# Performance work log

Measured on AMD Instinct MI355X. Metric: run time of the kernel, lower is better.

Reference implementation:

```python
import jax, jax.numpy as jnp
import numpy as np

BATCH, VOCAB = 256, 50257

def setup_inputs() -> dict:
    key = jax.random.key(0)
    k1, k2 = jax.random.split(key)
    logits = jax.random.normal(k1, (BATCH, VOCAB), dtype=jnp.float32) * 4.0  # LM-like logit spread
    temperature = jax.random.uniform(k2, (), dtype=jnp.float32, minval=0.5, maxval=1.5)
    return {"logits": logits, "temperature": temperature, "top_k": 50}


def reference(logits, temperature, top_k):
    # temperature scale (dividing by 1.0 is identical to the torch skip-branch)
    scaled = logits / temperature
    # top-k mask: keep exactly the k selected positions, -inf elsewhere
    top_vals, top_idx = jax.lax.top_k(scaled, top_k)          # [B, k]
    b = jnp.arange(scaled.shape[0])[:, None]                  # [B, 1]
    masked = jnp.full_like(scaled, -jnp.inf).at[b, top_idx].set(top_vals)
    # softmax + multinomial(num_samples=1) == categorical over masked logits
    key = jax.random.key(42)
    sampled = jax.random.categorical(key, masked, axis=-1)    # [B]
    return sampled
```

## Files before the change

### kernel.cpp

```cpp
#include <hip/hip_runtime.h>
#include <stdint.h>


#define VOCAB 50257
#define BATCH 256
#define NT 1024
#define NTF 256
#define NSEG 16
#define SEG4 786
#define CAP_SEG 64
#define NBINS 4096
#define HBINS 1024
#define BSHIFT 15
#define BCAP 256
#define CAND_CAP 2048
#define FILTER_VAL 4.0f
#define SPEC_VAL 10.0f

__device__ __forceinline__ uint32_t rotl32(uint32_t v, int r) {
  return (v << r) | (v >> (32 - r));
}

__device__ __forceinline__ void threefry2x32_42(uint32_t& x0, uint32_t& x1) {
  const uint32_t ks0 = 0u;
  const uint32_t ks1 = 42u;
  const uint32_t ks2 = ks0 ^ ks1 ^ 0x1BD11BDAu;
  x0 += ks0; x1 += ks1;
#define TF_R(r) { x0 += x1; x1 = rotl32(x1, (r)); x1 ^= x0; }
  TF_R(13) TF_R(15) TF_R(26) TF_R(6)
  x0 += ks1; x1 += ks2 + 1u;
  TF_R(17) TF_R(29) TF_R(16) TF_R(24)
  x0 += ks2; x1 += ks0 + 2u;
  TF_R(13) TF_R(15) TF_R(26) TF_R(6)
  x0 += ks0; x1 += ks1 + 3u;
  TF_R(17) TF_R(29) TF_R(16) TF_R(24)
  x0 += ks1; x1 += ks2 + 4u;
  TF_R(13) TF_R(15) TF_R(26) TF_R(6)
  x0 += ks2; x1 += ks0 + 5u;
#undef TF_R
}

__device__ __forceinline__ float gumbel_at(uint32_t flat) {
  uint32_t x0 = 0u, x1 = flat;
  threefry2x32_42(x0, x1);
  uint32_t bits = x0 ^ x1;
  uint32_t fb = (bits >> 9) | 0x3f800000u;
  float f = __uint_as_float(fb) - 1.0f;
  float u = fmaxf(f, 1.17549435e-38f);
  float t = (float)log((double)u);
  float g = (float)(-log((double)(-t)));
  return g;
}

__device__ __forceinline__ uint32_t fkey(float x) {
  uint32_t u = __float_as_uint(x);
  return (u & 0x80000000u) ? ~u : (u | 0x80000000u);
}

__device__ __forceinline__ float inv_fkey(uint32_t k) {
  uint32_t u = (k & 0x80000000u) ? (k ^ 0x80000000u) : ~k;
  return __uint_as_float(u);
}

extern "C" __global__ void __launch_bounds__(NTF)
filter_kernel(const float* __restrict__ logits,
              int* __restrict__ cnt,
              int* __restrict__ cand) {
  const int b = blockIdx.x;
  const int row = b >> 4;
  const int seg = b & 15;
  const int tid = threadIdx.x;
  const float* rowp = logits + (size_t)row * VOCAB;

  const int pc = (4 - (row & 3)) & 3;
  const int nv4 = (VOCAB - pc) >> 2;
  const int tailbase = pc + (nv4 << 2);
  const int tailc = VOCAB - tailbase;
  const float4* body = (const float4*)(rowp + pc);

  __shared__ int lcnt;
  if (tid == 0) lcnt = 0;
  __syncthreads();

  int* myc = cand + (b << 6);
  const int st = seg * SEG4;
  const int en = min(nv4, st + SEG4);
  for (int v = st + tid; v < en; v += NTF) {
    float4 x = body[v];
    int base = pc + (v << 2);
    if (x.x >= SPEC_VAL) { int p = atomicAdd(&lcnt, 1); if (p < CAP_SEG) myc[p] = base; }
    if (x.y >= SPEC_VAL) { int p = atomicAdd(&lcnt, 1); if (p < CAP_SEG) myc[p] = base + 1; }
    if (x.z >= SPEC_VAL) { int p = atomicAdd(&lcnt, 1); if (p < CAP_SEG) myc[p] = base + 2; }
    if (x.w >= SPEC_VAL) { int p = atomicAdd(&lcnt, 1); if (p < CAP_SEG) myc[p] = base + 3; }
  }
  if (seg == 0 && tid < pc) {
    if (rowp[tid] >= SPEC_VAL) { int p = atomicAdd(&lcnt, 1); if (p < CAP_SEG) myc[p] = tid; }
  }
  if (seg == NSEG - 1 && tid < tailc) {
    if (rowp[tailbase + tid] >= SPEC_VAL) {
      int p = atomicAdd(&lcnt, 1); if (p < CAP_SEG) myc[p] = tailbase + tid;
    }
  }
  __syncthreads();
  if (tid == 0) cnt[b] = lcnt;
}

extern "C" __global__ void __launch_bounds__(NTF)
refine_kernel(const float* __restrict__ logits,
              const float* __restrict__ temp_p,
              const int* __restrict__ topk_p,
              int* __restrict__ out,
              const int* __restrict__ cnt,
              const int* __restrict__ cand,
              int* __restrict__ flags) {
  const int row = blockIdx.x;
  const int tid = threadIdx.x;
  const int lane = tid & 63;
  const int wave = tid >> 6;

  __shared__ int scnt[NSEG], soff[NSEG];
  __shared__ int sh_total, sh_ok, sh_tb, sh_need, sh_bcnt;
  __shared__ unsigned ckey[CAND_CAP];
  __shared__ int cidx[CAND_CAP];
  __shared__ unsigned hist[HBINS];
  __shared__ unsigned bkey[BCAP];
  __shared__ int bidx[BCAP];
  __shared__ unsigned wtot[4], aboveWave[4];
  __shared__ float wbv[4];
  __shared__ int wbi[4];

  const int K = topk_p[0];
  const float temp = temp_p[0];

  if (tid < NSEG) scnt[tid] = cnt[(row << 4) + tid];
  if (tid == 0) { sh_ok = 0; sh_bcnt = 0; }
  for (int b = tid; b < HBINS; b += NTF) hist[b] = 0u;
  __syncthreads();
  if (tid == 0) {
    int acc = 0, ovf = 0;
    for (int s = 0; s < NSEG; ++s) {
      soff[s] = acc;
      if (scnt[s] > CAP_SEG) ovf = 1;
      acc += scnt[s];
    }
    sh_total = ovf ? -1 : acc;
  }
  __syncthreads();
  const int total = sh_total;

  if (!(total >= K && total <= CAND_CAP)) {
    if (tid == 0) flags[row] = 0;
    return;
  }

  {
    int s = tid >> 4, j0 = tid & 15;
    const int* src = cand + (((row << 4) + s) << 6);
    for (int j = j0; j < scnt[s]; j += 16) cidx[soff[s] + j] = src[j];
  }
  __syncthreads();

  const float* rowp = logits + (size_t)row * VOCAB;
  const uint32_t cutkey = fkey(SPEC_VAL / temp);
  for (int c = tid; c < total; c += NTF) {
    unsigned k = fkey(rowp[cidx[c]] / temp);
    ckey[c] = k;
    unsigned bin = min((unsigned)(HBINS - 1), (k - cutkey) >> BSHIFT);
    atomicAdd(&hist[bin], 1u);
  }
  __syncthreads();

  {
    unsigned p = hist[4 * tid] + hist[4 * tid + 1] + hist[4 * tid + 2] + hist[4 * tid + 3];
    unsigned vv = p;
    for (int off = 1; off < 64; off <<= 1) {
      unsigned o = (unsigned)__shfl_down((int)vv, off);
      if (lane + off < 64) vv += o;
    }
    if (lane == 0) wtot[wave] = vv;
    __syncthreads();
    if (tid == 0) {
      unsigned acc = 0;
      for (int w = 3; w >= 0; --w) { aboveWave[w] = acc; acc += wtot[w]; }
    }
    __syncthreads();
    unsigned above = aboveWave[wave] + (vv - p);
    if (above < (unsigned)K && above + p >= (unsigned)K) {
      int need = K - (int)above;
      for (int b = 3; b >= 0; --b) {
        unsigned c = hist[4 * tid + b];
        if (c >= (unsigned)need) { sh_tb = 4 * tid + b; sh_need = need; break; }
        need -= (int)c;
      }
    }
  }
  __syncthreads();
  const int tb = sh_tb;
  const int need = sh_need;

  for (int c = tid; c < total; c += NTF) {
    unsigned k = ckey[c];
    unsigned bin = min((unsigned)(HBINS - 1), (k - cutkey) >> BSHIFT);
    if ((int)bin == tb) {
      int p = atomicAdd(&sh_bcnt, 1);
      if (p < BCAP) { bkey[p] = k; bidx[p] = cidx[c]; }
    }
  }
  __syncthreads();
  const int m = sh_bcnt;
  if (m > BCAP) {
    if (tid == 0) flags[row] = 0;
    return;
  }

  float bestv = -__builtin_huge_valf();
  int besti = 0x7fffffff;

  if (tid < m) {
    const unsigned mk = bkey[tid];
    const int mi = bidx[tid];
    int rank = 0;
    for (int j = 0; j < m; ++j) {
      unsigned k = bkey[j];
      rank += (k > mk || (k == mk && bidx[j] < mi)) ? 1 : 0;
    }
    if (rank == need - 1) {
      sh_ok = (tb > 0 || mk > cutkey) ? 1 : 0;
    }
    if (rank < need) {
      float s = inv_fkey(mk);
      float v = s + gumbel_at((uint32_t)row * (uint32_t)VOCAB + (uint32_t)mi);
      if (v > bestv || (v == bestv && mi < besti)) { bestv = v; besti = mi; }
    }
  }

  for (int c = tid; c < total; c += NTF) {
    unsigned k = ckey[c];
    unsigned bin = min((unsigned)(HBINS - 1), (k - cutkey) >> BSHIFT);
    if ((int)bin > tb) {
      int mi = cidx[c];
      float s = inv_fkey(k);
      float v = s + gumbel_at((uint32_t)row * (uint32_t)VOCAB + (uint32_t)mi);
      if (v > bestv || (v == bestv && mi < besti)) { bestv = v; besti = mi; }
    }
  }
  __syncthreads();
  if (!sh_ok) {
    if (tid == 0) flags[row] = 0;
    return;
  }

  for (int off = 32; off > 0; off >>= 1) {
    float v2 = __shfl_down(bestv, off);
    int i2 = __shfl_down(besti, off);
    if (v2 > bestv || (v2 == bestv && i2 < besti)) { bestv = v2; besti = i2; }
  }
  if (lane == 0) { wbv[wave] = bestv; wbi[wave] = besti; }
  __syncthreads();
  if (tid == 0) {
    float bv = wbv[0]; int bi = wbi[0];
    for (int w = 1; w < 4; ++w) {
      if (wbv[w] > bv || (wbv[w] == bv && wbi[w] < bi)) { bv = wbv[w]; bi = wbi[w]; }
    }
    out[row] = bi;
    flags[row] = 1;
  }
}

extern "C" __global__ void __launch_bounds__(NT)
fallback_kernel(const float* __restrict__ logits,
                const float* __restrict__ temp_p,
                const int* __restrict__ topk_p,
                int* __restrict__ out,
                const int* __restrict__ flags) {
  const int row = blockIdx.x;
  if (flags[row]) return;

  const int tid = threadIdx.x;
  const float temp = temp_p[0];
  const int K = topk_p[0];
  const float* rowp = logits + (size_t)row * VOCAB;

  const int pc = (4 - (row & 3)) & 3;
  const int nv4 = (VOCAB - pc) >> 2;
  const int tailbase = pc + (nv4 << 2);
  const int tailc = VOCAB - tailbase;
  const float4* body = (const float4*)(rowp + pc);

  __shared__ unsigned hist[NBINS];
  __shared__ unsigned wtot[16];
  __shared__ unsigned aboveWave[16];
  __shared__ int sh_tb, sh_total, sh_cnt;
  __shared__ unsigned ckey[CAND_CAP];
  __shared__ int cidx[CAND_CAP];
  __shared__ float wbv[16];
  __shared__ int wbi[16];

  const int lane = tid & 63;
  const int wave = tid >> 6;

  float bestv = -__builtin_huge_valf();
  int besti = 0x7fffffff;

  uint32_t filt = fkey(FILTER_VAL);
  int tb = 0;
  for (;;) {
    for (int b = tid; b < NBINS; b += NT) hist[b] = 0u;
    __syncthreads();
    if (tid < pc) {
      uint32_t k = fkey(rowp[tid]);
      if (k >= filt) atomicAdd(&hist[k >> 20], 1u);
    }
    for (int w = tid; w < nv4; w += NT) {
      float4 x = body[w];
      uint32_t k0 = fkey(x.x), k1 = fkey(x.y), k2 = fkey(x.z), k3 = fkey(x.w);
      if (k0 >= filt) atomicAdd(&hist[k0 >> 20], 1u);
      if (k1 >= filt) atomicAdd(&hist[k1 >> 20], 1u);
      if (k2 >= filt) atomicAdd(&hist[k2 >> 20], 1u);
      if (k3 >= filt) atomicAdd(&hist[k3 >> 20], 1u);
    }
    if (tid < tailc) {
      uint32_t k = fkey(rowp[tailbase + tid]);
      if (k >= filt) atomicAdd(&hist[k >> 20], 1u);
    }
    __syncthreads();

    unsigned p = hist[4 * tid] + hist[4 * tid + 1] + hist[4 * tid + 2] + hist[4 * tid + 3];
    unsigned vv = p;
    for (int off = 1; off < 64; off <<= 1) {
      unsigned o = (unsigned)__shfl_down((int)vv, off);
      if (lane + off < 64) vv += o;
    }
    if (lane == 0) wtot[wave] = vv;
    __syncthreads();
    if (tid == 0) {
      unsigned acc = 0;
      for (int w = 15; w >= 0; --w) { aboveWave[w] = acc; acc += wtot[w]; }
      sh_total = (int)acc;
    }
    __syncthreads();
    unsigned above = aboveWave[wave] + (vv - p);
    if (above < (unsigned)K && above + p >= (unsigned)K) {
      int need = K - (int)above;
      for (int b = 3; b >= 0; --b) {
        unsigned c = hist[4 * tid + b];
        if (c >= (unsigned)need) { sh_tb = 4 * tid + b; break; }
        need -= (int)c;
      }
    }
    __syncthreads();
    if (sh_total >= K) { tb = sh_tb; break; }
    filt = 0u;
    __syncthreads();
  }

  const uint32_t cutk = (uint32_t)max(tb - 1, 0) << 20;
  if (tid == 0) sh_cnt = 0;
  __syncthreads();
  if (tid < pc) {
    if (fkey(rowp[tid]) >= cutk) {
      int p = atomicAdd(&sh_cnt, 1);
      if (p < CAND_CAP) cidx[p] = tid;
    }
  }
  for (int w = tid; w < nv4; w += NT) {
    float4 x = body[w];
    int base = pc + (w << 2);
    if (fkey(x.x) >= cutk) { int p = atomicAdd(&sh_cnt, 1); if (p < CAND_CAP) cidx[p] = base; }
    if (fkey(x.y) >= cutk) { int p = atomicAdd(&sh_cnt, 1); if (p < CAND_CAP) cidx[p] = base + 1; }
    if (fkey(x.z) >= cutk) { int p = atomicAdd(&sh_cnt, 1); if (p < CAND_CAP) cidx[p] = base + 2; }
    if (fkey(x.w) >= cutk) { int p = atomicAdd(&sh_cnt, 1); if (p < CAND_CAP) cidx[p] = base + 3; }
  }
  if (tid < tailc) {
    if (fkey(rowp[tailbase + tid]) >= cutk) {
      int p = atomicAdd(&sh_cnt, 1);
      if (p < CAND_CAP) cidx[p] = tailbase + tid;
    }
  }
  __syncthreads();
  const int C = min(sh_cnt, CAND_CAP);

  if (tid < C) {
    int idx = cidx[tid];
    float s = rowp[idx] / temp;
    ckey[tid] = fkey(s);
  }
  __syncthreads();

  if (tid < C) {
    const uint32_t mk = ckey[tid];
    const int mi = cidx[tid];
    int rank = 0;
    for (int j = 0; j < C; ++j) {
      uint32_t k = ckey[j];
      rank += (k > mk || (k == mk && cidx[j] < mi)) ? 1 : 0;
    }
    if (rank < K) {
      float s = rowp[mi] / temp;
      float v2 = s + gumbel_at((uint32_t)row * (uint32_t)VOCAB + (uint32_t)mi);
      bestv = v2; besti = mi;
    }
  }
  __syncthreads();

  for (int off = 32; off > 0; off >>= 1) {
    float v2 = __shfl_down(bestv, off);
    int i2 = __shfl_down(besti, off);
    if (v2 > bestv || (v2 == bestv && i2 < besti)) { bestv = v2; besti = i2; }
  }
  if (lane == 0) { wbv[wave] = bestv; wbi[wave] = besti; }
  __syncthreads();
  if (tid == 0) {
    float bv = wbv[0];
    int bi = wbi[0];
    for (int w = 1; w < 16; ++w) {
      if (wbv[w] > bv || (wbv[w] == bv && wbi[w] < bi)) { bv = wbv[w]; bi = wbi[w]; }
    }
    out[row] = bi;
  }
}

extern "C" void kernel_launch(void* const* d_in, const int* in_sizes, int n_in,
                              void* d_out, int out_size, void* d_ws, size_t ws_size,
                              hipStream_t stream) {
  const float* logits = (const float*)d_in[0];
  const float* temp_p = (const float*)d_in[1];
  const int* topk_p = (const int*)d_in[2];
  int* out = (int*)d_out;

  int* cnt = (int*)d_ws;
  int* cand = cnt + BATCH * NSEG;
  int* flags = cand + BATCH * NSEG * CAP_SEG;

  hipLaunchKernelGGL(filter_kernel, dim3(BATCH * NSEG), dim3(NTF), 0, stream,
                     logits, cnt, cand);
  hipLaunchKernelGGL(refine_kernel, dim3(BATCH), dim3(NTF), 0, stream,
                     logits, temp_p, topk_p, out, cnt, cand, flags);
  hipLaunchKernelGGL(fallback_kernel, dim3(BATCH), dim3(NT), 0, stream,
                     logits, temp_p, topk_p, out, flags);
}
```

Before: 95.80 us.

## Merge fallback into refine kernel and store candidate values alongside indices

The filter kernel now writes each candidate's logit value next to its index, so the refine step no longer gathers from the full logits row. The fallback path is folded into the refine kernel, which now runs with 1024 threads and uses a 1024-bin histogram with one bin per thread. This removes the third kernel launch and the flags buffer. In exchange the refine blocks are larger and carry more shared memory on every row, and the filter kernel writes twice as much to the workspace.

```diff
diff --git a/kernel.cpp b/kernel.cpp
--- a/kernel.cpp
+++ b/kernel.cpp
@@ -65,7 +65,8 @@
 extern "C" __global__ void __launch_bounds__(NTF)
 filter_kernel(const float* __restrict__ logits,
               int* __restrict__ cnt,
-              int* __restrict__ cand) {
+              int* __restrict__ cand_idx,
+              float* __restrict__ cand_val) {
   const int b = blockIdx.x;
   const int row = b >> 4;
   const int seg = b & 15;
@@ -82,59 +83,62 @@
   if (tid == 0) lcnt = 0;
   __syncthreads();
 
-  int* myc = cand + (b << 6);
+  int* myi = cand_idx + (b << 6);
+  float* myv = cand_val + (b << 6);
   const int st = seg * SEG4;
   const int en = min(nv4, st + SEG4);
   for (int v = st + tid; v < en; v += NTF) {
     float4 x = body[v];
     int base = pc + (v << 2);
-    if (x.x >= SPEC_VAL) { int p = atomicAdd(&lcnt, 1); if (p < CAP_SEG) myc[p] = base; }
-    if (x.y >= SPEC_VAL) { int p = atomicAdd(&lcnt, 1); if (p < CAP_SEG) myc[p] = base + 1; }
-    if (x.z >= SPEC_VAL) { int p = atomicAdd(&lcnt, 1); if (p < CAP_SEG) myc[p] = base + 2; }
-    if (x.w >= SPEC_VAL) { int p = atomicAdd(&lcnt, 1); if (p < CAP_SEG) myc[p] = base + 3; }
+    if (x.x >= SPEC_VAL) { int p = atomicAdd(&lcnt, 1); if (p < CAP_SEG) { myi[p] = base;     myv[p] = x.x; } }
+    if (x.y >= SPEC_VAL) { int p = atomicAdd(&lcnt, 1); if (p < CAP_SEG) { myi[p] = base + 1; myv[p] = x.y; } }
+    if (x.z >= SPEC_VAL) { int p = atomicAdd(&lcnt, 1); if (p < CAP_SEG) { myi[p] = base + 2; myv[p] = x.z; } }
+    if (x.w >= SPEC_VAL) { int p = atomicAdd(&lcnt, 1); if (p < CAP_SEG) { myi[p] = base + 3; myv[p] = x.w; } }
   }
   if (seg == 0 && tid < pc) {
-    if (rowp[tid] >= SPEC_VAL) { int p = atomicAdd(&lcnt, 1); if (p < CAP_SEG) myc[p] = tid; }
+    float x = rowp[tid];
+    if (x >= SPEC_VAL) { int p = atomicAdd(&lcnt, 1); if (p < CAP_SEG) { myi[p] = tid; myv[p] = x; } }
   }
   if (seg == NSEG - 1 && tid < tailc) {
-    if (rowp[tailbase + tid] >= SPEC_VAL) {
-      int p = atomicAdd(&lcnt, 1); if (p < CAP_SEG) myc[p] = tailbase + tid;
+    float x = rowp[tailbase + tid];
+    if (x >= SPEC_VAL) {
+      int p = atomicAdd(&lcnt, 1); if (p < CAP_SEG) { myi[p] = tailbase + tid; myv[p] = x; }
     }
   }
   __syncthreads();
   if (tid == 0) cnt[b] = lcnt;
 }
 
-extern "C" __global__ void __launch_bounds__(NTF)
+extern "C" __global__ void __launch_bounds__(NT)
 refine_kernel(const float* __restrict__ logits,
               const float* __restrict__ temp_p,
               const int* __restrict__ topk_p,
               int* __restrict__ out,
               const int* __restrict__ cnt,
-              const int* __restrict__ cand,
-              int* __restrict__ flags) {
+              const int* __restrict__ cand_idx,
+              const float* __restrict__ cand_val) {
   const int row = blockIdx.x;
   const int tid = threadIdx.x;
   const int lane = tid & 63;
   const int wave = tid >> 6;
 
-  __shared__ int scnt[NSEG], soff[NSEG];
-  __shared__ int sh_total, sh_ok, sh_tb, sh_need, sh_bcnt;
+  __shared__ unsigned hist[NBINS];
   __shared__ unsigned ckey[CAND_CAP];
   __shared__ int cidx[CAND_CAP];
-  __shared__ unsigned hist[HBINS];
+  __shared__ int scnt[NSEG], soff[NSEG];
+  __shared__ int sh_total, sh_ok, sh_tb, sh_need, sh_bcnt, sh_cnt;
   __shared__ unsigned bkey[BCAP];
   __shared__ int bidx[BCAP];
-  __shared__ unsigned wtot[4], aboveWave[4];
-  __shared__ float wbv[4];
-  __shared__ int wbi[4];
+  __shared__ unsigned wtot[16], aboveWave[16];
+  __shared__ float wbv[16];
+  __shared__ int wbi[16];
 
   const int K = topk_p[0];
   const float temp = temp_p[0];
 
   if (tid < NSEG) scnt[tid] = cnt[(row << 4) + tid];
   if (tid == 0) { sh_ok = 0; sh_bcnt = 0; }
-  for (int b = tid; b < HBINS; b += NTF) hist[b] = 0u;
+  if (tid < HBINS) hist[tid] = 0u;
   __syncthreads();
   if (tid == 0) {
     int acc = 0, ovf = 0;
@@ -148,275 +152,242 @@
   __syncthreads();
   const int total = sh_total;
 
-  if (!(total >= K && total <= CAND_CAP)) {
-    if (tid == 0) flags[row] = 0;
-    return;
-  }
-
-  {
-    int s = tid >> 4, j0 = tid & 15;
-    const int* src = cand + (((row << 4) + s) << 6);
-    for (int j = j0; j < scnt[s]; j += 16) cidx[soff[s] + j] = src[j];
-  }
-  __syncthreads();
-
-  const float* rowp = logits + (size_t)row * VOCAB;
+  int ok = (total >= K && total <= CAND_CAP) ? 1 : 0;
   const uint32_t cutkey = fkey(SPEC_VAL / temp);
-  for (int c = tid; c < total; c += NTF) {
-    unsigned k = fkey(rowp[cidx[c]] / temp);
-    ckey[c] = k;
-    unsigned bin = min((unsigned)(HBINS - 1), (k - cutkey) >> BSHIFT);
-    atomicAdd(&hist[bin], 1u);
-  }
-  __syncthreads();
-
-  {
-    unsigned p = hist[4 * tid] + hist[4 * tid + 1] + hist[4 * tid + 2] + hist[4 * tid + 3];
-    unsigned vv = p;
-    for (int off = 1; off < 64; off <<= 1) {
-      unsigned o = (unsigned)__shfl_down((int)vv, off);
-      if (lane + off < 64) vv += o;
-    }
-    if (lane == 0) wtot[wave] = vv;
-    __syncthreads();
-    if (tid == 0) {
-      unsigned acc = 0;
-      for (int w = 3; w >= 0; --w) { aboveWave[w] = acc; acc += wtot[w]; }
-    }
-    __syncthreads();
-    unsigned above = aboveWave[wave] + (vv - p);
-    if (above < (unsigned)K && above + p >= (unsigned)K) {
-      int need = K - (int)above;
-      for (int b = 3; b >= 0; --b) {
-        unsigned c = hist[4 * tid + b];
-        if (c >= (unsigned)need) { sh_tb = 4 * tid + b; sh_need = need; break; }
-        need -= (int)c;
-      }
-    }
-  }
-  __syncthreads();
-  const int tb = sh_tb;
-  const int need = sh_need;
-
-  for (int c = tid; c < total; c += NTF) {
-    unsigned k = ckey[c];
-    unsigned bin = min((unsigned)(HBINS - 1), (k - cutkey) >> BSHIFT);
-    if ((int)bin == tb) {
-      int p = atomicAdd(&sh_bcnt, 1);
-      if (p < BCAP) { bkey[p] = k; bidx[p] = cidx[c]; }
-    }
-  }
-  __syncthreads();
-  const int m = sh_bcnt;
-  if (m > BCAP) {
-    if (tid == 0) flags[row] = 0;
-    return;
-  }
 
   float bestv = -__builtin_huge_valf();
   int besti = 0x7fffffff;
 
-  if (tid < m) {
-    const unsigned mk = bkey[tid];
-    const int mi = bidx[tid];
-    int rank = 0;
-    for (int j = 0; j < m; ++j) {
-      unsigned k = bkey[j];
-      rank += (k > mk || (k == mk && bidx[j] < mi)) ? 1 : 0;
-    }
-    if (rank == need - 1) {
-      sh_ok = (tb > 0 || mk > cutkey) ? 1 : 0;
-    }
-    if (rank < need) {
-      float s = inv_fkey(mk);
-      float v = s + gumbel_at((uint32_t)row * (uint32_t)VOCAB + (uint32_t)mi);
-      if (v > bestv || (v == bestv && mi < besti)) { bestv = v; besti = mi; }
-    }
-  }
-
-  for (int c = tid; c < total; c += NTF) {
-    unsigned k = ckey[c];
-    unsigned bin = min((unsigned)(HBINS - 1), (k - cutkey) >> BSHIFT);
-    if ((int)bin > tb) {
-      int mi = cidx[c];
-      float s = inv_fkey(k);
-      float v = s + gumbel_at((uint32_t)row * (uint32_t)VOCAB + (uint32_t)mi);
-      if (v > bestv || (v == bestv && mi < besti)) { bestv = v; besti = mi; }
-    }
-  }
-  __syncthreads();
-  if (!sh_ok) {
-    if (tid == 0) flags[row] = 0;
+  if (ok) {
+    {
+      int s = tid >> 6, j0 = tid & 63;
+      const int* srci = cand_idx + (((row << 4) + s) << 6);
+      const float* srcv = cand_val + (((row << 4) + s) << 6);
+      for (int j = j0; j < scnt[s]; j += 64) {
+        int o = soff[s] + j;
+        cidx[o] = srci[j];
+        ckey[o] = fkey(srcv[j] / temp);
+      }
+    }
+    __syncthreads();
+    for (int c = tid; c < total; c += NT) {
+      unsigned bin = min((unsigned)(HBINS - 1), (ckey[c] - cutkey) >> BSHIFT);
+      atomicAdd(&hist[bin], 1u);
+    }
+    __syncthreads();
+    {
+      unsigned p = hist[tid];
+      unsigned vv = p;
+      for (int off = 1; off < 64; off <<= 1) {
+        unsigned o = (unsigned)__shfl_down((int)vv, off);
+        if (lane + off < 64) vv += o;
+      }
+      if (lane == 0) wtot[wave] = vv;
+      __syncthreads();
+      if (tid == 0) {
+        unsigned acc = 0;
+        for (int w = 15; w >= 0; --w) { aboveWave[w] = acc; acc += wtot[w]; }
+      }
+      __syncthreads();
+      unsigned above = aboveWave[wave] + (vv - p);
+      if (above < (unsigned)K && above + p >= (unsigned)K) {
+        sh_tb = tid; sh_need = K - (int)above;
+      }
+    }
+    __syncthreads();
+    const int tb = sh_tb;
+    const int need = sh_need;
+
+    for (int c = tid; c < total; c += NT) {
+      unsigned k = ckey[c];
+      unsigned bin = min((unsigned)(HBINS - 1), (k - cutkey) >> BSHIFT);
+      if ((int)bin == tb) {
+        int p = atomicAdd(&sh_bcnt, 1);
+        if (p < BCAP) { bkey[p] = k; bidx[p] = cidx[c]; }
+      }
+    }
+    __syncthreads();
+    const int m = sh_bcnt;
+    if (m > BCAP) ok = 0;
+
+    if (ok) {
+      if (tid < m) {
+        const unsigned mk = bkey[tid];
+        const int mi = bidx[tid];
+        int rank = 0;
+        for (int j = 0; j < m; ++j) {
+          unsigned k = bkey[j];
+          rank += (k > mk || (k == mk && bidx[j] < mi)) ? 1 : 0;
+        }
+        if (rank == need - 1) {
+          sh_ok = (tb > 0 || mk > cutkey) ? 1 : 0;
+        }
+        if (rank < need) {
+          float s = inv_fkey(mk);
+          float v = s + gumbel_at((uint32_t)row * (uint32_t)VOCAB + (uint32_t)mi);
+          if (v > bestv || (v == bestv && mi < besti)) { bestv = v; besti = mi; }
+        }
+      }
+      for (int c = tid; c < total; c += NT) {
+        unsigned k = ckey[c];
+        unsigned bin = min((unsigned)(HBINS - 1), (k - cutkey) >> BSHIFT);
+        if ((int)bin > tb) {
+          int mi = cidx[c];
+          float s = inv_fkey(k);
+          float v = s + gumbel_at((uint32_t)row * (uint32_t)VOCAB + (uint32_t)mi);
+          if (v > bestv || (v == bestv && mi < besti)) { bestv = v; besti = mi; }
+        }
+      }
+      __syncthreads();
+      if (!sh_ok) ok = 0;
+    }
+  }
+
+  if (ok) {
+    for (int off = 32; off > 0; off >>= 1) {
+      float v2 = __shfl_down(bestv, off);
+      int i2 = __shfl_down(besti, off);
+      if (v2 > bestv || (v2 == bestv && i2 < besti)) { bestv = v2; besti = i2; }
+    }
+    if (lane == 0) { wbv[wave] = bestv; wbi[wave] = besti; }
+    __syncthreads();
+    if (tid == 0) {
+      float bv = wbv[0]; int bi = wbi[0];
+      for (int w = 1; w < 16; ++w) {
+        if (wbv[w] > bv || (wbv[w] == bv && wbi[w] < bi)) { bv = wbv[w]; bi = wbi[w]; }
+      }
+      out[row] = bi;
+    }
     return;
   }
 
-  for (int off = 32; off > 0; off >>= 1) {
-    float v2 = __shfl_down(bestv, off);
-    int i2 = __shfl_down(besti, off);
-    if (v2 > bestv || (v2 == bestv && i2 < besti)) { bestv = v2; besti = i2; }
-  }
-  if (lane == 0) { wbv[wave] = bestv; wbi[wave] = besti; }
-  __syncthreads();
-  if (tid == 0) {
-    float bv = wbv[0]; int bi = wbi[0];
-    for (int w = 1; w < 4; ++w) {
-      if (wbv[w] > bv || (wbv[w] == bv && wbi[w] < bi)) { bv = wbv[w]; bi = wbi[w]; }
-    }
-    out[row] = bi;
-    flags[row] = 1;
-  }
-}
-
-extern "C" __global__ void __launch_bounds__(NT)
-fallback_kernel(const float* __restrict__ logits,
-                const float* __restrict__ temp_p,
-                const int* __restrict__ topk_p,
-                int* __restrict__ out,
-                const int* __restrict__ flags) {
-  const int row = blockIdx.x;
-  if (flags[row]) return;
-
-  const int tid = threadIdx.x;
-  const float temp = temp_p[0];
-  const int K = topk_p[0];
-  const float* rowp = logits + (size_t)row * VOCAB;
-
-  const int pc = (4 - (row & 3)) & 3;
-  const int nv4 = (VOCAB - pc) >> 2;
-  const int tailbase = pc + (nv4 << 2);
-  const int tailc = VOCAB - tailbase;
-  const float4* body = (const float4*)(rowp + pc);
-
-  __shared__ unsigned hist[NBINS];
-  __shared__ unsigned wtot[16];
-  __shared__ unsigned aboveWave[16];
-  __shared__ int sh_tb, sh_total, sh_cnt;
-  __shared__ unsigned ckey[CAND_CAP];
-  __shared__ int cidx[CAND_CAP];
-  __shared__ float wbv[16];
-  __shared__ int wbi[16];
-
-  const int lane = tid & 63;
-  const int wave = tid >> 6;
-
-  float bestv = -__builtin_huge_valf();
-  int besti = 0x7fffffff;
-
-  uint32_t filt = fkey(FILTER_VAL);
-  int tb = 0;
-  for (;;) {
-    for (int b = tid; b < NBINS; b += NT) hist[b] = 0u;
+  {
+    const float* rowp = logits + (size_t)row * VOCAB;
+    const int pc = (4 - (row & 3)) & 3;
+    const int nv4 = (VOCAB - pc) >> 2;
+    const int tailbase = pc + (nv4 << 2);
+    const int tailc = VOCAB - tailbase;
+    const float4* body = (const float4*)(rowp + pc);
+
+    bestv = -__builtin_huge_valf();
+    besti = 0x7fffffff;
+
+    uint32_t filt = fkey(FILTER_VAL);
+    int tb = 0;
+    for (;;) {
+      for (int b = tid; b < NBINS; b += NT) hist[b] = 0u;
+      __syncthreads();
+      if (tid < pc) {
+        uint32_t k = fkey(rowp[tid]);
+        if (k >= filt) atomicAdd(&hist[k >> 20], 1u);
+      }
+      for (int w = tid; w < nv4; w += NT) {
+        float4 x = body[w];
+        uint32_t k0 = fkey(x.x), k1 = fkey(x.y), k2 = fkey(x.z), k3 = fkey(x.w);
+        if (k0 >= filt) atomicAdd(&hist[k0 >> 20], 1u);
+        if (k1 >= filt) atomicAdd(&hist[k1 >> 20], 1u);
+        if (k2 >= filt) atomicAdd(&hist[k2 >> 20], 1u);
+        if (k3 >= filt) atomicAdd(&hist[k3 >> 20], 1u);
+      }
+      if (tid < tailc) {
+        uint32_t k = fkey(rowp[tailbase + tid]);
+        if (k >= filt) atomicAdd(&hist[k >> 20], 1u);
+      }
+      __syncthreads();
+
+      unsigned p = hist[4 * tid] + hist[4 * tid + 1] + hist[4 * tid + 2] + hist[4 * tid + 3];
+      unsigned vv = p;
+      for (int off = 1; off < 64; off <<= 1) {
+        unsigned o = (unsigned)__shfl_down((int)vv, off);
+        if (lane + off < 64) vv += o;
+      }
+      if (lane == 0) wtot[wave] = vv;
+      __syncthreads();
+      if (tid == 0) {
+        unsigned acc = 0;
+        for (int w = 15; w >= 0; --w) { aboveWave[w] = acc; acc += wtot[w]; }
+        sh_total = (int)acc;
+      }
+      __syncthreads();
+      unsigned above = aboveWave[wave] + (vv - p);
+      if (above < (unsigned)K && above + p >= (unsigned)K) {
+        int need = K - (int)above;
+        for (int b = 3; b >= 0; --b) {
+          unsigned c = hist[4 * tid + b];
+          if (c >= (unsigned)need) { sh_tb = 4 * tid + b; break; }
+          need -= (int)c;
+        }
+      }
+      __syncthreads();
+      if (sh_total >= K) { tb = sh_tb; break; }
+      filt = 0u;
+      __syncthreads();
+    }
+
+    const uint32_t cutk = (uint32_t)max(tb - 1, 0) << 20;
+    if (tid == 0) sh_cnt = 0;
     __syncthreads();
     if (tid < pc) {
-      uint32_t k = fkey(rowp[tid]);
-      if (k >= filt) atomicAdd(&hist[k >> 20], 1u);
+      if (fkey(rowp[tid]) >= cutk) {
+        int p = atomicAdd(&sh_cnt, 1);
+        if (p < CAND_CAP) cidx[p] = tid;
+      }
     }
     for (int w = tid; w < nv4; w += NT) {
       float4 x = body[w];
-      uint32_t k0 = fkey(x.x), k1 = fkey(x.y), k2 = fkey(x.z), k3 = fkey(x.w);
-      if (k0 >= filt) atomicAdd(&hist[k0 >> 20], 1u);
-      if (k1 >= filt) atomicAdd(&hist[k1 >> 20], 1u);
-      if (k2 >= filt) atomicAdd(&hist[k2 >> 20], 1u);
-      if (k3 >= filt) atomicAdd(&hist[k3 >> 20], 1u);
+      int base = pc + (w << 2);
+      if (fkey(x.x) >= cutk) { int p = atomicAdd(&sh_cnt, 1); if (p < CAND_CAP) cidx[p] = base; }
+      if (fkey(x.y) >= cutk) { int p = atomicAdd(&sh_cnt, 1); if (p < CAND_CAP) cidx[p] = base + 1; }
+      if (fkey(x.z) >= cutk) { int p = atomicAdd(&sh_cnt, 1); if (p < CAND_CAP) cidx[p] = base + 2; }
+      if (fkey(x.w) >= cutk) { int p = atomicAdd(&sh_cnt, 1); if (p < CAND_CAP) cidx[p] = base + 3; }
     }
     if (tid < tailc) {
-      uint32_t k = fkey(rowp[tailbase + tid]);
-      if (k >= filt) atomicAdd(&hist[k >> 20], 1u);
-    }
-    __syncthreads();
-
-    unsigned p = hist[4 * tid] + hist[4 * tid + 1] + hist[4 * tid + 2] + hist[4 * tid + 3];
-    unsigned vv = p;
-    for (int off = 1; off < 64; off <<= 1) {
-      unsigned o = (unsigned)__shfl_down((int)vv, off);
-      if (lane + off < 64) vv += o;
-    }
-    if (lane == 0) wtot[wave] = vv;
+      if (fkey(rowp[tailbase + tid]) >= cutk) {
+        int p = atomicAdd(&sh_cnt, 1);
+        if (p < CAND_CAP) cidx[p] = tailbase + tid;
+      }
+    }
+    __syncthreads();
+    const int C = min(sh_cnt, CAND_CAP);
+
+    if (tid < C) {
+      int idx = cidx[tid];
+      float s = rowp[idx] / temp;
+      ckey[tid] = fkey(s);
+    }
+    __syncthreads();
+
+    if (tid < C) {
+      const uint32_t mk = ckey[tid];
+      const int mi = cidx[tid];
+      int rank = 0;
+      for (int j = 0; j < C; ++j) {
+        uint32_t k = ckey[j];
+        rank += (k > mk || (k == mk && cidx[j] < mi)) ? 1 : 0;
+      }
+      if (rank < K) {
+        float s = rowp[mi] / temp;
+        float v2 = s + gumbel_at((uint32_t)row * (uint32_t)VOCAB + (uint32_t)mi);
+        bestv = v2; besti = mi;
+      }
+    }
+    __syncthreads();
+
+    for (int off = 32; off > 0; off >>= 1) {
+      float v2 = __shfl_down(bestv, off);
+      int i2 = __shfl_down(besti, off);
+      if (v2 > bestv || (v2 == bestv && i2 < besti)) { bestv = v2; besti = i2; }
+    }
+    if (lane == 0) { wbv[wave] = bestv; wbi[wave] = besti; }
     __syncthreads();
     if (tid == 0) {
-      unsigned acc = 0;
-      for (int w = 15; w >= 0; --w) { aboveWave[w] = acc; acc += wtot[w]; }
-      sh_total = (int)acc;
-    }
-    __syncthreads();
-    unsigned above = aboveWave[wave] + (vv - p);
-    if (above < (unsigned)K && above + p >= (unsigned)K) {
-      int need = K - (int)above;
-      for (int b = 3; b >= 0; --b) {
-        unsigned c = hist[4 * tid + b];
-        if (c >= (unsigned)need) { sh_tb = 4 * tid + b; break; }
-        need -= (int)c;
-      }
-    }
-    __syncthreads();
-    if (sh_total >= K) { tb = sh_tb; break; }
-    filt = 0u;
-    __syncthreads();
-  }
-
-  const uint32_t cutk = (uint32_t)max(tb - 1, 0) << 20;
-  if (tid == 0) sh_cnt = 0;
-  __syncthreads();
-  if (tid < pc) {
-    if (fkey(rowp[tid]) >= cutk) {
-      int p = atomicAdd(&sh_cnt, 1);
-      if (p < CAND_CAP) cidx[p] = tid;
-    }
-  }
-  for (int w = tid; w < nv4; w += NT) {
-    float4 x = body[w];
-    int base = pc + (w << 2);
-    if (fkey(x.x) >= cutk) { int p = atomicAdd(&sh_cnt, 1); if (p < CAND_CAP) cidx[p] = base; }
-    if (fkey(x.y) >= cutk) { int p = atomicAdd(&sh_cnt, 1); if (p < CAND_CAP) cidx[p] = base + 1; }
-    if (fkey(x.z) >= cutk) { int p = atomicAdd(&sh_cnt, 1); if (p < CAND_CAP) cidx[p] = base + 2; }
-    if (fkey(x.w) >= cutk) { int p = atomicAdd(&sh_cnt, 1); if (p < CAND_CAP) cidx[p] = base + 3; }
-  }
-  if (tid < tailc) {
-    if (fkey(rowp[tailbase + tid]) >= cutk) {
-      int p = atomicAdd(&sh_cnt, 1);
-      if (p < CAND_CAP) cidx[p] = tailbase + tid;
-    }
-  }
-  __syncthreads();
-  const int C = min(sh_cnt, CAND_CAP);
-
-  if (tid < C) {
-    int idx = cidx[tid];
-    float s = rowp[idx] / temp;
-    ckey[tid] = fkey(s);
-  }
-  __syncthreads();
-
-  if (tid < C) {
-    const uint32_t mk = ckey[tid];
-    const int mi = cidx[tid];
-    int rank = 0;
-    for (int j = 0; j < C; ++j) {
-      uint32_t k = ckey[j];
-      rank += (k > mk || (k == mk && cidx[j] < mi)) ? 1 : 0;
-    }
-    if (rank < K) {
-      float s = rowp[mi] / temp;
-      float v2 = s + gumbel_at((uint32_t)row * (uint32_t)VOCAB + (uint32_t)mi);
-      bestv = v2; besti = mi;
-    }
-  }
-  __syncthreads();
-
-  for (int off = 32; off > 0; off >>= 1) {
-    float v2 = __shfl_down(bestv, off);
-    int i2 = __shfl_down(besti, off);
-    if (v2 > bestv || (v2 == bestv && i2 < besti)) { bestv = v2; besti = i2; }
-  }
-  if (lane == 0) { wbv[wave] = bestv; wbi[wave] = besti; }
-  __syncthreads();
-  if (tid == 0) {
-    float bv = wbv[0];
-    int bi = wbi[0];
-    for (int w = 1; w < 16; ++w) {
-      if (wbv[w] > bv || (wbv[w] == bv && wbi[w] < bi)) { bv = wbv[w]; bi = wbi[w]; }
-    }
-    out[row] = bi;
+      float bv = wbv[0];
+      int bi = wbi[0];
+      for (int w = 1; w < 16; ++w) {
+        if (wbv[w] > bv || (wbv[w] == bv && wbi[w] < bi)) { bv = wbv[w]; bi = wbi[w]; }
+      }
+      out[row] = bi;
+    }
   }
 }
 
@@ -429,13 +400,11 @@
   int* out = (int*)d_out;
 
   int* cnt = (int*)d_ws;
-  int* cand = cnt + BATCH * NSEG;
-  int* flags = cand + BATCH * NSEG * CAP_SEG;
+  int* cand_idx = cnt + BATCH * NSEG;
+  float* cand_val = (float*)(cand_idx + BATCH * NSEG * CAP_SEG);
 
   hipLaunchKernelGGL(filter_kernel, dim3(BATCH * NSEG), dim3(NTF), 0, stream,
-                     logits, cnt, cand);
-  hipLaunchKernelGGL(refine_kernel, dim3(BATCH), dim3(NTF), 0, stream,
-                     logits, temp_p, topk_p, out, cnt, cand, flags);
-  hipLaunchKernelGGL(fallback_kernel, dim3(BATCH), dim3(NT), 0, stream,
-                     logits, temp_p, topk_p, out, flags);
-}
+                     logits, cnt, cand_idx, cand_val);
+  hipLaunchKernelGGL(refine_kernel, dim3(BATCH), dim3(NT), 0, stream,
+                     logits, temp_p, topk_p, out, cnt, cand_idx, cand_val);
+}
```

Result: no change. 94.49 us (-1.4%).
